# Kernel tuning notes

Hardware: AMD Instinct MI355X
Metric: run time of the kernel (lower is better)

Reference implementation:

```python
import jax, jax.numpy as jnp
import numpy as np

N = 8000          # num_nodes
DEG = 8           # avg out-degree of random road graph
B = 32            # batch size
INPUT_DIM = 2
UNITS = 64        # rnn_units
K = 2             # max_diffusion_step
NUM_SUPPORTS = 2  # dual_random_walk


def _spmm(rows, cols, vals, x):
    # sparse @ dense: y[r] += vals * x[c] for each coo entry (r, c)
    return jax.ops.segment_sum(vals[:, None] * x[cols], rows, num_segments=N)


def _gconv(inputs, state, supports, W, b):
    # Chebyshev-style diffusion conv, faithful to GCONV.forward layout
    Bsz = inputs.shape[0]
    x = jnp.concatenate([inputs.reshape(Bsz, N, -1), state.reshape(Bsz, N, -1)], axis=2)
    F = x.shape[2]                                   # input_dim + units
    x0 = jnp.transpose(x, (1, 2, 0)).reshape(N, F * Bsz)
    xs = [x0]
    for rows, cols, vals in supports:
        x1 = _spmm(rows, cols, vals, x0)
        xs.append(x1)
        xk2, xk1 = x0, x1
        for _ in range(2, K + 1):
            x2 = 2.0 * _spmm(rows, cols, vals, xk1) - xk2
            xs.append(x2)
            xk2, xk1 = xk1, x2
    M = len(xs)                                      # num_matrices = 2*K+1
    xc = jnp.stack(xs).reshape(M, N, F, Bsz)
    xc = jnp.transpose(xc, (3, 1, 2, 0)).reshape(Bsz * N, F * M)
    out = xc @ W + b
    return out.reshape(Bsz, N * W.shape[1])


def setup_inputs() -> dict:
    rng = np.random.default_rng(0)
    rows = np.repeat(np.arange(N, dtype=np.int32), DEG)
    cols = rng.integers(0, N, size=N * DEG).astype(np.int32)
    vals = rng.uniform(0.5, 1.5, size=N * DEG).astype(np.float32)
    # random-walk normalization: rw(A) = D^-1 A ; supports are rw(A).T and rw(A.T).T
    rsum = np.zeros(N, np.float32); np.add.at(rsum, rows, vals)
    csum = np.zeros(N, np.float32); np.add.at(csum, cols, vals)
    rinv = np.where(rsum > 0, 1.0 / np.maximum(rsum, 1e-12), 0.0).astype(np.float32)
    cinv = np.where(csum > 0, 1.0 / np.maximum(csum, 1e-12), 0.0).astype(np.float32)
    # support0 = (D^-1 A)^T: entry (cols[i], rows[i]) = vals[i] * rinv[rows[i]]
    s0_rows, s0_cols, s0_vals = cols, rows, (vals * rinv[rows]).astype(np.float32)
    # support1 = (D_T^-1 A^T)^T: entry (rows[i], cols[i]) = vals[i] * cinv[cols[i]]
    s1_rows, s1_cols, s1_vals = rows, cols, (vals * cinv[cols]).astype(np.float32)

    key = jax.random.key(0)
    k1, k2, k3, k4 = jax.random.split(key, 4)
    F = INPUT_DIM + UNITS
    M = NUM_SUPPORTS * K + 1
    xavier = lambda k, shape: jax.random.normal(k, shape, jnp.float32) * np.float32(np.sqrt(2.0 / (shape[0] + shape[1])))
    W_ru = xavier(k1, (F * M, 2 * UNITS))
    b_ru = jnp.ones((2 * UNITS,), jnp.float32)    # bias_start=1.0
    W_c = xavier(k2, (F * M, UNITS))
    b_c = jnp.zeros((UNITS,), jnp.float32)        # bias_start=0.0
    inputs = jax.random.normal(k3, (B, N * INPUT_DIM), jnp.float32)
    hx = jax.random.normal(k4, (B, N * UNITS), jnp.float32)
    return {
        "inputs": inputs, "hx": hx,
        "W_ru": W_ru, "b_ru": b_ru, "W_c": W_c, "b_c": b_c,
        "s0_rows": jnp.asarray(s0_rows), "s0_cols": jnp.asarray(s0_cols), "s0_vals": jnp.asarray(s0_vals),
        "s1_rows": jnp.asarray(s1_rows), "s1_cols": jnp.asarray(s1_cols), "s1_vals": jnp.asarray(s1_vals),
    }


def reference(inputs, hx, W_ru, b_ru, W_c, b_c,
              s0_rows, s0_cols, s0_vals, s1_rows, s1_cols, s1_vals):
    supports = [(s0_rows, s0_cols, s0_vals), (s1_rows, s1_cols, s1_vals)]
    value = jax.nn.sigmoid(_gconv(inputs, hx, supports, W_ru, b_ru))
    value = value.reshape(-1, N, 2 * UNITS)
    r = value[..., :UNITS].reshape(-1, N * UNITS)
    u = value[..., UNITS:].reshape(-1, N * UNITS)
    c = jnp.tanh(_gconv(inputs, r * hx, supports, W_c, b_c))
    return u * hx + (1.0 - u) * c
```

## Files before the change

kernel.cpp:

```cpp
#include <hip/hip_runtime.h>
#include <stdint.h>

typedef unsigned short u16;
typedef unsigned int   u32;

typedef __attribute__((ext_vector_type(8))) short bf16x8;
typedef __attribute__((ext_vector_type(4))) float f32x4;

#define NNODES 8000
#define BSZ    32
#define UNITS  64
#define EDG    64000
#define ROWCH  288
#define NODECH 1440
#define NODEU16 11520
#define KLIN   384
#define NSTEPS 12
#define HXROW  512000
#define INROW  16000

__device__ __forceinline__ u32 f2bf(float f){
    u32 u = __float_as_uint(f);
    return (u + 0x7FFFu + ((u >> 16) & 1u)) >> 16;
}
__device__ __forceinline__ float bfu(u16 s){ return __uint_as_float(((u32)s) << 16); }
__device__ __forceinline__ float lo16(u32 u){ return __uint_as_float(u << 16); }
__device__ __forceinline__ float hi16(u32 u){ return __uint_as_float(u & 0xFFFF0000u); }
__device__ __forceinline__ float sigm(float x){ return 1.f / (1.f + __expf(-x)); }

#define GLDS(gsrc, ldst) \
    __builtin_amdgcn_global_load_lds((const __attribute__((address_space(1))) void*)(gsrc), \
                                     (__attribute__((address_space(3))) void*)(ldst), 16, 0, 0)

__global__ void hist_k(const int* __restrict__ rows, int* __restrict__ counts){
    int e = blockIdx.x * 256 + threadIdx.x;
    if (e < EDG) atomicAdd(&counts[rows[e]], 1);
}

__global__ __launch_bounds__(256) void scan_k(const int* __restrict__ counts,
                                              int* __restrict__ row_ptr,
                                              int* __restrict__ cursor){
    __shared__ int part[256];
    int t = threadIdx.x;
    int s = 0;
    for (int i = 0; i < 32; ++i){ int r = t*32 + i; if (r < NNODES) s += counts[r]; }
    part[t] = s;
    __syncthreads();
    if (t == 0){
        int run = 0;
        for (int i = 0; i < 256; ++i){ int v = part[i]; part[i] = run; run += v; }
    }
    __syncthreads();
    int run = part[t];
    for (int i = 0; i < 32; ++i){
        int r = t*32 + i;
        if (r < NNODES){ row_ptr[r] = run; cursor[r] = run; run += counts[r]; }
    }
    if (t == 255) row_ptr[NNODES] = run;
}

__global__ void scatter_k(const int* __restrict__ rows, const int* __restrict__ cols,
                          const float* __restrict__ vals, int* __restrict__ cursor,
                          int* __restrict__ cs, float* __restrict__ vs){
    int e = blockIdx.x * 256 + threadIdx.x;
    if (e < EDG){
        int r = rows[e];
        int slot = atomicAdd(&cursor[r], 1);
        cs[slot] = cols[e];
        vs[slot] = vals[e];
    }
}

__global__ void prep_w_k(const float* __restrict__ W_ru, const float* __restrict__ W_c,
                         u16* __restrict__ Wt_ru, u16* __restrict__ Wt_c){
    int id = blockIdx.x * 256 + threadIdx.x;
    if (id < 128*KLIN){
        int j = id & 7;
        int cell = id >> 3;
        int col = cell & 127;
        int sq = cell >> 7;
        int kl = sq*8 + j;
        int m = kl / 72, fp = kl - m*72;
        u16 v = 0;
        if (m < 5 && fp < 66){
            float w;
            if (m == 0)      w = W_ru[(fp*5 + 0)*128 + col] - W_ru[(fp*5 + 2)*128 + col] - W_ru[(fp*5 + 4)*128 + col];
            else if (m == 2) w = 2.f * W_ru[(fp*5 + 2)*128 + col];
            else if (m == 4) w = 2.f * W_ru[(fp*5 + 4)*128 + col];
            else             w = W_ru[(fp*5 + m)*128 + col];
            v = (u16)f2bf(w);
        }
        Wt_ru[id] = v;
    }
    int id2 = id - 128*KLIN;
    if (id2 >= 0 && id2 < 64*KLIN){
        int j = id2 & 7;
        int cell = id2 >> 3;
        int col = cell & 63;
        int sq = cell >> 6;
        int kl = sq*8 + j;
        int m = kl / 72, fp = kl - m*72;
        u16 v = 0;
        if (m < 5 && fp < 66){
            float w;
            if (m == 0)      w = W_c[(fp*5 + 0)*64 + col] - W_c[(fp*5 + 2)*64 + col] - W_c[(fp*5 + 4)*64 + col];
            else if (m == 2) w = 2.f * W_c[(fp*5 + 2)*64 + col];
            else if (m == 4) w = 2.f * W_c[(fp*5 + 4)*64 + col];
            else             w = W_c[(fp*5 + m)*64 + col];
            v = (u16)f2bf(w);
        }
        Wt_c[id2] = v;
    }
}

__global__ __launch_bounds__(256) void build_x0_k(const float* __restrict__ inputs,
                                                  const float* __restrict__ hx,
                                                  u16* __restrict__ Xu){
    __shared__ float sl[32*72];
    int n = blockIdx.x, t = threadIdx.x;
    #pragma unroll
    for (int i = 0; i < 8; ++i){
        int idx = t + i*256;
        int b = idx >> 6, f = idx & 63;
        sl[b*72 + 2 + f] = hx[b*HXROW + n*64 + f];
    }
    if (t < 64){
        int b = t >> 1, d = t & 1;
        sl[b*72 + d] = inputs[b*INROW + n*2 + d];
    }
    if (t < 192){
        int b = t / 6, k = t - b*6;
        sl[b*72 + 66 + k] = 0.f;
    }
    __syncthreads();
    #pragma unroll
    for (int i = 0; i < 2; ++i){
        int j = t + i*256;
        if (j < ROWCH){
            int b = j & 31, s = j >> 5;
            const float* p = &sl[b*72 + s*8];
            uint4 o;
            o.x = f2bf(p[0]) | (f2bf(p[1]) << 16);
            o.y = f2bf(p[2]) | (f2bf(p[3]) << 16);
            o.z = f2bf(p[4]) | (f2bf(p[5]) << 16);
            o.w = f2bf(p[6]) | (f2bf(p[7]) << 16);
            ((uint4*)Xu)[(size_t)n*NODECH + j] = o;
        }
    }
}

__device__ __forceinline__ void acc8(float* a, uint4 q, float v){
    a[0] += v*lo16(q.x); a[1] += v*hi16(q.x);
    a[2] += v*lo16(q.y); a[3] += v*hi16(q.y);
    a[4] += v*lo16(q.z); a[5] += v*hi16(q.z);
    a[6] += v*lo16(q.w); a[7] += v*hi16(q.w);
}
__device__ __forceinline__ uint4 pack8(const float* a){
    uint4 o;
    o.x = f2bf(a[0]) | (f2bf(a[1]) << 16);
    o.y = f2bf(a[2]) | (f2bf(a[3]) << 16);
    o.z = f2bf(a[4]) | (f2bf(a[5]) << 16);
    o.w = f2bf(a[6]) | (f2bf(a[7]) << 16);
    return o;
}

__global__ __launch_bounds__(288) void diff1_k(u16* __restrict__ Xu,
                                               const int* __restrict__ rp,
                                               const int* __restrict__ c0, const float* __restrict__ v0,
                                               const int* __restrict__ c1, const float* __restrict__ v1){
    int t = threadIdx.x;
    if (t >= ROWCH) return;
    int n = blockIdx.x;
    const uint4* xb = (const uint4*)Xu;
    float a[8] = {0,0,0,0,0,0,0,0};
    float d[8] = {0,0,0,0,0,0,0,0};
    {
        uint4 q[8]; float vv[8];
        #pragma unroll
        for (int i = 0; i < 8; ++i){
            int c = c1[n*8 + i]; vv[i] = v1[n*8 + i];
            q[i] = xb[(size_t)c*NODECH + t];
        }
        #pragma unroll
        for (int i = 0; i < 8; ++i) acc8(d, q[i], vv[i]);
    }
    int e = rp[n], end = rp[n+1];
    for (; e + 8 <= end; e += 8){
        uint4 q[8]; float vv[8];
        #pragma unroll
        for (int i = 0; i < 8; ++i){
            int c = c0[e+i]; vv[i] = v0[e+i];
            q[i] = xb[(size_t)c*NODECH + t];
        }
        #pragma unroll
        for (int i = 0; i < 8; ++i) acc8(a, q[i], vv[i]);
    }
    for (; e < end; ++e){
        int c = c0[e]; float v = v0[e];
        acc8(a, xb[(size_t)c*NODECH + t], v);
    }
    ((uint4*)Xu)[(size_t)n*NODECH + 1*ROWCH + t] = pack8(a);
    ((uint4*)Xu)[(size_t)n*NODECH + 3*ROWCH + t] = pack8(d);
}

__global__ __launch_bounds__(288) void diff2_k(u16* __restrict__ Xu,
                                               const int* __restrict__ rp,
                                               const int* __restrict__ c0, const float* __restrict__ v0,
                                               const int* __restrict__ c1, const float* __restrict__ v1){
    int t = threadIdx.x;
    if (t >= ROWCH) return;
    int n = blockIdx.x;
    const uint4* xb = (const uint4*)Xu;
    float a[8] = {0,0,0,0,0,0,0,0};
    float d[8] = {0,0,0,0,0,0,0,0};
    {
        uint4 q[8]; float vv[8];
        #pragma unroll
        for (int i = 0; i < 8; ++i){
            int c = c1[n*8 + i]; vv[i] = v1[n*8 + i];
            q[i] = xb[(size_t)c*NODECH + 3*ROWCH + t];
        }
        #pragma unroll
        for (int i = 0; i < 8; ++i) acc8(d, q[i], vv[i]);
    }
    int e = rp[n], end = rp[n+1];
    for (; e + 8 <= end; e += 8){
        uint4 q[8]; float vv[8];
        #pragma unroll
        for (int i = 0; i < 8; ++i){
            int c = c0[e+i]; vv[i] = v0[e+i];
            q[i] = xb[(size_t)c*NODECH + 1*ROWCH + t];
        }
        #pragma unroll
        for (int i = 0; i < 8; ++i) acc8(a, q[i], vv[i]);
    }
    for (; e < end; ++e){
        int c = c0[e]; float v = v0[e];
        acc8(a, xb[(size_t)c*NODECH + 1*ROWCH + t], v);
    }
    ((uint4*)Xu)[(size_t)n*NODECH + 2*ROWCH + t] = pack8(a);
    ((uint4*)Xu)[(size_t)n*NODECH + 4*ROWCH + t] = pack8(d);
}

__global__ __launch_bounds__(512) void gemm_ru_k(
        const u16* Xu,
        const u16* __restrict__ WtS,
        const float* __restrict__ b_ru,
        u16* __restrict__ U, u16* X0st){
    __shared__ u16 Bs[2][4096];
    const int t = threadIdx.x;
    const int lane = t & 63, w = t >> 6;
    const int node = blockIdx.x*8 + w;
    const int cIn = lane & 15, q = lane >> 4;
    const size_t noff = (size_t)node * NODEU16;
    const u16* Xn = Xu + noff;

    f32x4 acc[2][8];
    const f32x4 z4 = {0.f,0.f,0.f,0.f};
    #pragma unroll
    for (int rt = 0; rt < 2; ++rt)
        #pragma unroll
        for (int ct = 0; ct < 8; ++ct) acc[rt][ct] = z4;

    GLDS(WtS + t*8, &Bs[0][w*512]);
    bf16x8 A0 = *(const bf16x8*)&Xn[(size_t)(q*32 + cIn)*8];
    bf16x8 A1 = *(const bf16x8*)&Xn[(size_t)(q*32 + 16 + cIn)*8];
    __syncthreads();

    int cur = 0;
    #pragma unroll
    for (int st = 0; st < NSTEPS; ++st){
        bf16x8 p0, p1;
        if (st + 1 < NSTEPS){
            GLDS(WtS + (size_t)(st+1)*4096 + t*8, &Bs[cur^1][w*512]);
            p0 = *(const bf16x8*)&Xn[(size_t)(((st+1)*4 + q)*32 + cIn)*8];
            p1 = *(const bf16x8*)&Xn[(size_t)(((st+1)*4 + q)*32 + 16 + cIn)*8];
        }
        bf16x8 cb[8];
        #pragma unroll
        for (int ct = 0; ct < 8; ++ct)
            cb[ct] = *(const bf16x8*)&Bs[cur][(q*128 + ct*16 + cIn)*8];
        #pragma unroll
        for (int ct = 0; ct < 8; ++ct){
            acc[0][ct] = __builtin_amdgcn_mfma_f32_16x16x32_bf16(A0, cb[ct], acc[0][ct], 0,0,0);
            acc[1][ct] = __builtin_amdgcn_mfma_f32_16x16x32_bf16(A1, cb[ct], acc[1][ct], 0,0,0);
        }
        __syncthreads();
        if (st + 1 < NSTEPS){ A0 = p0; A1 = p1; }
        cur ^= 1;
    }

    #pragma unroll
    for (int ct = 0; ct < 8; ++ct){
        int col = ct*16 + cIn;
        float bias = b_ru[col];
        #pragma unroll
        for (int rt = 0; rt < 2; ++rt){
            int b0 = rt*16 + q*4;
            f32x4 d = acc[rt][ct];
            if (ct < 4){
                int fp = 2 + col;
                int s = fp >> 3, off = fp & 7;
                #pragma unroll
                for (int i = 0; i < 4; ++i){
                    size_t idx = noff + (size_t)(s*32 + b0 + i)*8 + off;
                    float h = bfu(X0st[idx]);
                    float rg = sigm(d[i] + bias);
                    X0st[idx] = (u16)f2bf(rg * h);
                }
            } else {
                uint2 pk;
                float v0 = sigm(d[0] + bias), v1 = sigm(d[1] + bias);
                float v2 = sigm(d[2] + bias), v3 = sigm(d[3] + bias);
                pk.x = f2bf(v0) | (f2bf(v1) << 16);
                pk.y = f2bf(v2) | (f2bf(v3) << 16);
                *(uint2*)&U[(size_t)node*2048 + (col - 64)*32 + b0] = pk;
            }
        }
    }
}

__global__ __launch_bounds__(512) void gemm_c_k(
        const u16* __restrict__ Xu,
        const u16* __restrict__ WtS,
        const float* __restrict__ b_c, const float* __restrict__ hx,
        const u16* __restrict__ U, float* __restrict__ out){
    __shared__ u16 Bs[2][2048];
    const int t = threadIdx.x;
    const int lane = t & 63, w = t >> 6;
    const int node = blockIdx.x*8 + w;
    const int cIn = lane & 15, q = lane >> 4;
    const size_t noff = (size_t)node * NODEU16;
    const u16* Xn = Xu + noff;

    f32x4 acc[2][4];
    const f32x4 z4 = {0.f,0.f,0.f,0.f};
    #pragma unroll
    for (int rt = 0; rt < 2; ++rt)
        #pragma unroll
        for (int ct = 0; ct < 4; ++ct) acc[rt][ct] = z4;

    if (t < 256) GLDS(WtS + t*8, &Bs[0][w*512]);
    bf16x8 A0 = *(const bf16x8*)&Xn[(size_t)(q*32 + cIn)*8];
    bf16x8 A1 = *(const bf16x8*)&Xn[(size_t)(q*32 + 16 + cIn)*8];
    __syncthreads();

    int cur = 0;
    #pragma unroll
    for (int st = 0; st < NSTEPS; ++st){
        bf16x8 p0, p1;
        if (st + 1 < NSTEPS){
            if (t < 256) GLDS(WtS + (size_t)(st+1)*2048 + t*8, &Bs[cur^1][w*512]);
            p0 = *(const bf16x8*)&Xn[(size_t)(((st+1)*4 + q)*32 + cIn)*8];
            p1 = *(const bf16x8*)&Xn[(size_t)(((st+1)*4 + q)*32 + 16 + cIn)*8];
        }
        bf16x8 cb[4];
        #pragma unroll
        for (int ct = 0; ct < 4; ++ct)
            cb[ct] = *(const bf16x8*)&Bs[cur][(q*64 + ct*16 + cIn)*8];
        #pragma unroll
        for (int ct = 0; ct < 4; ++ct){
            acc[0][ct] = __builtin_amdgcn_mfma_f32_16x16x32_bf16(A0, cb[ct], acc[0][ct], 0,0,0);
            acc[1][ct] = __builtin_amdgcn_mfma_f32_16x16x32_bf16(A1, cb[ct], acc[1][ct], 0,0,0);
        }
        __syncthreads();
        if (st + 1 < NSTEPS){ A0 = p0; A1 = p1; }
        cur ^= 1;
    }

    #pragma unroll
    for (int ct = 0; ct < 4; ++ct){
        int col = ct*16 + cIn;
        float bias = b_c[col];
        #pragma unroll
        for (int rt = 0; rt < 2; ++rt){
            int b0 = rt*16 + q*4;
            f32x4 d = acc[rt][ct];
            uint2 up = *(const uint2*)&U[(size_t)node*2048 + col*32 + b0];
            float uu[4] = { lo16(up.x), hi16(up.x), lo16(up.y), hi16(up.y) };
            #pragma unroll
            for (int i = 0; i < 4; ++i){
                float c = tanhf(d[i] + bias);
                size_t gi = (size_t)(b0 + i)*HXROW + node*64 + col;
                float h = hx[gi];
                out[gi] = uu[i]*h + (1.f - uu[i])*c;
            }
        }
    }
}

extern "C" void kernel_launch(void* const* d_in, const int* in_sizes, int n_in,
                              void* d_out, int out_size, void* d_ws, size_t ws_size,
                              hipStream_t stream){
    const float* inputs = (const float*)d_in[0];
    const float* hx     = (const float*)d_in[1];
    const float* W_ru   = (const float*)d_in[2];
    const float* b_ru   = (const float*)d_in[3];
    const float* W_c    = (const float*)d_in[4];
    const float* b_c    = (const float*)d_in[5];
    const int*   s0r    = (const int*)d_in[6];
    const int*   s0c    = (const int*)d_in[7];
    const float* s0v    = (const float*)d_in[8];
    const int*   s1c    = (const int*)d_in[10];
    const float* s1v    = (const float*)d_in[11];
    float* out = (float*)d_out;

    char* ws = (char*)d_ws;
    size_t off = 0;
    auto alloc = [&](size_t bytes) -> char* {
        char* p = ws + off;
        off += (bytes + 255) & ~(size_t)255;
        return p;
    };
    const size_t XU_BYTES = (size_t)NNODES * NODEU16 * 2;
    u16* Xu   = (u16*)alloc(XU_BYTES + 4096);
    u16* U    = (u16*)alloc((size_t)NNODES*2048*2);
    u16* WtRU = (u16*)alloc((size_t)128*KLIN*2);
    u16* WtC  = (u16*)alloc((size_t)64*KLIN*2);
    int* counts  = (int*)alloc((size_t)NNODES*4);
    int* row_ptr = (int*)alloc((size_t)(NNODES+1)*4);
    int* cursor  = (int*)alloc((size_t)NNODES*4);
    int*   cols_s = (int*)alloc((size_t)EDG*4);
    float* vals_s = (float*)alloc((size_t)EDG*4);
    (void)ws_size; (void)in_sizes; (void)n_in; (void)out_size;

    hipMemsetAsync(counts, 0, (size_t)NNODES*4, stream);
    hipMemsetAsync((char*)Xu + XU_BYTES, 0, 4096, stream);
    hist_k<<<250, 256, 0, stream>>>(s0r, counts);
    scan_k<<<1, 256, 0, stream>>>(counts, row_ptr, cursor);
    scatter_k<<<250, 256, 0, stream>>>(s0r, s0c, s0v, cursor, cols_s, vals_s);

    prep_w_k<<<288, 256, 0, stream>>>(W_ru, W_c, WtRU, WtC);
    build_x0_k<<<NNODES, 256, 0, stream>>>(inputs, hx, Xu);

    diff1_k<<<NNODES, 288, 0, stream>>>(Xu, row_ptr, cols_s, vals_s, s1c, s1v);
    diff2_k<<<NNODES, 288, 0, stream>>>(Xu, row_ptr, cols_s, vals_s, s1c, s1v);

    gemm_ru_k<<<NNODES/8, 512, 0, stream>>>(Xu, WtRU, b_ru, U, Xu);

    diff1_k<<<NNODES, 288, 0, stream>>>(Xu, row_ptr, cols_s, vals_s, s1c, s1v);
    diff2_k<<<NNODES, 288, 0, stream>>>(Xu, row_ptr, cols_s, vals_s, s1c, s1v);

    gemm_c_k<<<NNODES/8, 512, 0, stream>>>(Xu, WtC, b_c, hx, U, out);
}
```

Measured before the change: 664.8 us.

## Stage weights in large LDS chunks to drop per-step barriers in GEMMs

Both GEMM kernels now load the weight matrix into shared memory in large chunks (all of it for the c-gate, two halves for ru) instead of double-buffering one K-step at a time. This removes the per-step __syncthreads and lets the unrolled loop issue A-operand loads freely. It raises LDS usage to 48KB per block, which may lower occupancy, and drops the explicit software prefetch of A operands.

```diff
diff --git a/kernel.cpp b/kernel.cpp
--- a/kernel.cpp
+++ b/kernel.cpp
@@ -247,7 +247,7 @@
         const u16* __restrict__ WtS,
         const float* __restrict__ b_ru,
         u16* __restrict__ U, u16* X0st){
-    __shared__ u16 Bs[2][4096];
+    __shared__ u16 Bs[24576];
     const int t = threadIdx.x;
     const int lane = t & 63, w = t >> 6;
     const int node = blockIdx.x*8 + w;
@@ -262,32 +262,35 @@
         #pragma unroll
         for (int ct = 0; ct < 8; ++ct) acc[rt][ct] = z4;
 
-    GLDS(WtS + t*8, &Bs[0][w*512]);
-    bf16x8 A0 = *(const bf16x8*)&Xn[(size_t)(q*32 + cIn)*8];
-    bf16x8 A1 = *(const bf16x8*)&Xn[(size_t)(q*32 + 16 + cIn)*8];
+    #pragma unroll
+    for (int i = 0; i < 6; ++i)
+        GLDS(WtS + (size_t)(i*512 + t)*8, &Bs[(i*512 + t)*8]);
     __syncthreads();
 
-    int cur = 0;
-    #pragma unroll
-    for (int st = 0; st < NSTEPS; ++st){
-        bf16x8 p0, p1;
-        if (st + 1 < NSTEPS){
-            GLDS(WtS + (size_t)(st+1)*4096 + t*8, &Bs[cur^1][w*512]);
-            p0 = *(const bf16x8*)&Xn[(size_t)(((st+1)*4 + q)*32 + cIn)*8];
-            p1 = *(const bf16x8*)&Xn[(size_t)(((st+1)*4 + q)*32 + 16 + cIn)*8];
-        }
-        bf16x8 cb[8];
-        #pragma unroll
-        for (int ct = 0; ct < 8; ++ct)
-            cb[ct] = *(const bf16x8*)&Bs[cur][(q*128 + ct*16 + cIn)*8];
-        #pragma unroll
-        for (int ct = 0; ct < 8; ++ct){
-            acc[0][ct] = __builtin_amdgcn_mfma_f32_16x16x32_bf16(A0, cb[ct], acc[0][ct], 0,0,0);
-            acc[1][ct] = __builtin_amdgcn_mfma_f32_16x16x32_bf16(A1, cb[ct], acc[1][ct], 0,0,0);
-        }
-        __syncthreads();
-        if (st + 1 < NSTEPS){ A0 = p0; A1 = p1; }
-        cur ^= 1;
+    #pragma unroll
+    for (int h = 0; h < 2; ++h){
+        if (h == 1){
+            __syncthreads();
+            #pragma unroll
+            for (int i = 0; i < 6; ++i)
+                GLDS(WtS + (size_t)(3072 + i*512 + t)*8, &Bs[(i*512 + t)*8]);
+            __syncthreads();
+        }
+        #pragma unroll
+        for (int ls = 0; ls < 6; ++ls){
+            const int st = h*6 + ls;
+            bf16x8 A0 = *(const bf16x8*)&Xn[(size_t)((st*4 + q)*32 + cIn)*8];
+            bf16x8 A1 = *(const bf16x8*)&Xn[(size_t)((st*4 + q)*32 + 16 + cIn)*8];
+            bf16x8 cb[8];
+            #pragma unroll
+            for (int ct = 0; ct < 8; ++ct)
+                cb[ct] = *(const bf16x8*)&Bs[((ls*4 + q)*128 + ct*16 + cIn)*8];
+            #pragma unroll
+            for (int ct = 0; ct < 8; ++ct){
+                acc[0][ct] = __builtin_amdgcn_mfma_f32_16x16x32_bf16(A0, cb[ct], acc[0][ct], 0,0,0);
+                acc[1][ct] = __builtin_amdgcn_mfma_f32_16x16x32_bf16(A1, cb[ct], acc[1][ct], 0,0,0);
+            }
+        }
     }
 
     #pragma unroll
@@ -304,9 +307,9 @@
                 #pragma unroll
                 for (int i = 0; i < 4; ++i){
                     size_t idx = noff + (size_t)(s*32 + b0 + i)*8 + off;
-                    float h = bfu(X0st[idx]);
+                    float h2 = bfu(X0st[idx]);
                     float rg = sigm(d[i] + bias);
-                    X0st[idx] = (u16)f2bf(rg * h);
+                    X0st[idx] = (u16)f2bf(rg * h2);
                 }
             } else {
                 uint2 pk;
@@ -325,7 +328,7 @@
         const u16* __restrict__ WtS,
         const float* __restrict__ b_c, const float* __restrict__ hx,
         const u16* __restrict__ U, float* __restrict__ out){
-    __shared__ u16 Bs[2][2048];
+    __shared__ u16 Bs[24576];
     const int t = threadIdx.x;
     const int lane = t & 63, w = t >> 6;
     const int node = blockIdx.x*8 + w;
@@ -340,32 +343,24 @@
         #pragma unroll
         for (int ct = 0; ct < 4; ++ct) acc[rt][ct] = z4;
 
-    if (t < 256) GLDS(WtS + t*8, &Bs[0][w*512]);
-    bf16x8 A0 = *(const bf16x8*)&Xn[(size_t)(q*32 + cIn)*8];
-    bf16x8 A1 = *(const bf16x8*)&Xn[(size_t)(q*32 + 16 + cIn)*8];
+    #pragma unroll
+    for (int i = 0; i < 6; ++i)
+        GLDS(WtS + (size_t)(i*512 + t)*8, &Bs[(i*512 + t)*8]);
     __syncthreads();
 
-    int cur = 0;
     #pragma unroll
     for (int st = 0; st < NSTEPS; ++st){
-        bf16x8 p0, p1;
-        if (st + 1 < NSTEPS){
-            if (t < 256) GLDS(WtS + (size_t)(st+1)*2048 + t*8, &Bs[cur^1][w*512]);
-            p0 = *(const bf16x8*)&Xn[(size_t)(((st+1)*4 + q)*32 + cIn)*8];
-            p1 = *(const bf16x8*)&Xn[(size_t)(((st+1)*4 + q)*32 + 16 + cIn)*8];
-        }
+        bf16x8 A0 = *(const bf16x8*)&Xn[(size_t)((st*4 + q)*32 + cIn)*8];
+        bf16x8 A1 = *(const bf16x8*)&Xn[(size_t)((st*4 + q)*32 + 16 + cIn)*8];
         bf16x8 cb[4];
         #pragma unroll
         for (int ct = 0; ct < 4; ++ct)
-            cb[ct] = *(const bf16x8*)&Bs[cur][(q*64 + ct*16 + cIn)*8];
+            cb[ct] = *(const bf16x8*)&Bs[((st*4 + q)*64 + ct*16 + cIn)*8];
         #pragma unroll
         for (int ct = 0; ct < 4; ++ct){
             acc[0][ct] = __builtin_amdgcn_mfma_f32_16x16x32_bf16(A0, cb[ct], acc[0][ct], 0,0,0);
             acc[1][ct] = __builtin_amdgcn_mfma_f32_16x16x32_bf16(A1, cb[ct], acc[1][ct], 0,0,0);
         }
-        __syncthreads();
-        if (st + 1 < NSTEPS){ A0 = p0; A1 = p1; }
-        cur ^= 1;
     }
 
     #pragma unroll
```

New measurement: 675.6 us. No clear change (+1.6%).
